# Optimization experiments

Measured on AMD Instinct MI355X. Metric: run time of the kernel, lower is better.

The kernel has to match this reference:

```python
import jax, jax.numpy as jnp
import numpy as np
from jax import lax

B, T, H = 32768, 64, 16
VOCAB_USER = 600001
VOCAB_LAUNCH = 3


def setup_inputs() -> dict:
    key = jax.random.key(0)
    ks = jax.random.split(key, 10)
    s = 1.0 / np.sqrt(H)
    return {
        "user_id": jax.random.randint(ks[0], (B,), 0, VOCAB_USER),
        "launch_seq": jax.random.randint(ks[1], (B, T), 0, VOCAB_LAUNCH),
        "user_emb": jax.random.normal(ks[2], (VOCAB_USER, H), dtype=jnp.float32),
        "launch_emb": jax.random.normal(ks[3], (VOCAB_LAUNCH, H), dtype=jnp.float32),
        "W_ih": jax.random.uniform(ks[4], (3 * H, H), jnp.float32, -s, s),
        "W_hh": jax.random.uniform(ks[5], (3 * H, H), jnp.float32, -s, s),
        "b_ih": jax.random.uniform(ks[6], (3 * H,), jnp.float32, -s, s),
        "b_hh": jax.random.uniform(ks[7], (3 * H,), jnp.float32, -s, s),
        "fc_W": jax.random.uniform(ks[8], (1, 2 * H), jnp.float32, -s, s),
        "fc_b": jax.random.uniform(ks[9], (1,), jnp.float32, -s, s),
    }


def reference(user_id, launch_seq, user_emb, launch_emb, W_ih, W_hh, b_ih, b_hh, fc_W, fc_b):
    u = user_emb[user_id]                      # (B, H)
    x = launch_emb[launch_seq]                 # (B, T, H)
    # precompute input contributions to the gates for all timesteps
    gx_all = jnp.einsum('bth,gh->btg', x, W_ih) + b_ih  # (B, T, 3H)

    def step(h, gx):
        gh = h @ W_hh.T + b_hh                 # (B, 3H)
        r = jax.nn.sigmoid(gx[:, :H] + gh[:, :H])
        z = jax.nn.sigmoid(gx[:, H:2 * H] + gh[:, H:2 * H])
        n = jnp.tanh(gx[:, 2 * H:] + r * gh[:, 2 * H:])
        h_new = (1.0 - z) * n + z * h
        return h_new, h_new

    h0 = jnp.zeros((x.shape[0], H), dtype=x.dtype)
    _, hs = lax.scan(step, h0, jnp.swapaxes(gx_all, 0, 1))  # hs: (T, B, H)
    pooled = jnp.mean(hs, axis=0)              # (B, H)
    fc_in = jnp.concatenate([u, pooled], axis=1)  # (B, 2H)
    return fc_in @ fc_W.T + fc_b               # (B, 1)
```

## Files before the change

kernel.cpp:

```cpp
#include <hip/hip_runtime.h>
#include <hip/hip_bf16.h>
#include <string.h>


#define NBLK 1024

typedef __attribute__((ext_vector_type(8)))  short    short8;
typedef __attribute__((ext_vector_type(16))) float    floatx16;
typedef __attribute__((ext_vector_type(4)))  unsigned uintx4;

static __device__ __forceinline__ float fexp2(float x) { return __builtin_amdgcn_exp2f(x); }
static __device__ __forceinline__ float frcp(float x)  { return __builtin_amdgcn_rcpf(x); }
static __device__ __forceinline__ unsigned short bfrne(float f) {
    union { __hip_bfloat16 b; unsigned short u; } cv; cv.b = __float2bfloat16(f); return cv.u;
}
static __device__ __forceinline__ float bf2f(unsigned short u) {
    unsigned v = ((unsigned)u) << 16; float f; memcpy(&f, &v, 4); return f;
}
static __device__ __forceinline__ unsigned pkbf(float a, float b) {
    return (unsigned)bfrne(a) | ((unsigned)bfrne(b) << 16);
}
static __device__ __forceinline__ float sel3(int c, float a0, float a1, float a2) {
    return c == 0 ? a0 : (c == 1 ? a1 : a2);
}

__global__ __launch_bounds__(64) void gru_mfma32(
    const int* __restrict__ user_id,
    const int* __restrict__ launch_seq,
    const float* __restrict__ user_emb,
    const float* __restrict__ launch_emb,
    const float* __restrict__ W_ih,
    const float* __restrict__ W_hh,
    const float* __restrict__ b_ih,
    const float* __restrict__ b_hh,
    const float* __restrict__ fc_W,
    const float* __restrict__ fc_b,
    float* __restrict__ out)
{
    constexpr float L  = 1.4426950408889634f;
    constexpr float L2 = 2.8853900817779268f;

    __shared__ float gxlut[144];

    const int tid  = threadIdx.x;
    const int n    = tid & 31;
    const int half = tid >> 5;
    const int d1o  = 4 * half;
    const long long sampBase = (long long)blockIdx.x * 32;

    unsigned pk[4];
    {
        const int* sp = launch_seq + (sampBase + n) * 64;
        #pragma unroll
        for (int w = 0; w < 4; ++w) {
            unsigned p = 0;
            #pragma unroll
            for (int j = 0; j < 4; ++j) {
                int4 v = ((const int4*)sp)[w * 4 + j];
                p |= ((unsigned)v.x & 3u) << (2 * (4 * j + 0));
                p |= ((unsigned)v.y & 3u) << (2 * (4 * j + 1));
                p |= ((unsigned)v.z & 3u) << (2 * (4 * j + 2));
                p |= ((unsigned)v.w & 3u) << (2 * (4 * j + 3));
            }
            pk[w] = p;
        }
    }

    for (int idx = tid; idx < 144; idx += 64) {
        int s = idx / 48, g = idx - s * 48;
        float dot = b_ih[g];
        #pragma unroll
        for (int k = 0; k < 16; ++k)
            dot = fmaf(W_ih[g * 16 + k], launch_emb[s * 16 + k], dot);
        int gate = g >> 4, dim = g & 15;
        gxlut[(gate * 3 + s) * 16 + dim] =
            (g < 32) ? (-L * (dot + b_hh[g])) : (L2 * dot);
    }

    short8 Arzh, Arzl, Anh, Anl;
    {
        auto split8 = [&](const float* w, short8& Hi, short8& Lo) {
            uintx4 hi, lo;
            #pragma unroll
            for (int p = 0; p < 4; ++p) {
                unsigned short h0 = bfrne(w[2 * p]), h1 = bfrne(w[2 * p + 1]);
                hi[p] = (unsigned)h0 | ((unsigned)h1 << 16);
                lo[p] = pkbf(w[2 * p] - bf2f(h0), w[2 * p + 1] - bf2f(h1));
            }
            Hi = __builtin_bit_cast(short8, hi);
            Lo = __builtin_bit_cast(short8, lo);
        };
        float w[8];
        const float* rowrz = W_hh + n * 16;
        float4 a = *(const float4*)(rowrz + d1o);
        float4 b = *(const float4*)(rowrz + d1o + 8);
        w[0] = -L * a.x; w[1] = -L * a.y; w[2] = -L * a.z; w[3] = -L * a.w;
        w[4] = -L * b.x; w[5] = -L * b.y; w[6] = -L * b.z; w[7] = -L * b.w;
        split8(w, Arzh, Arzl);
        if (n < 16) {
            const float* rown = W_hh + (32 + n) * 16;
            a = *(const float4*)(rown + d1o);
            b = *(const float4*)(rown + d1o + 8);
            w[0] = L2 * a.x; w[1] = L2 * a.y; w[2] = L2 * a.z; w[3] = L2 * a.w;
            w[4] = L2 * b.x; w[5] = L2 * b.y; w[6] = L2 * b.z; w[7] = L2 * b.w;
        } else {
            #pragma unroll
            for (int j = 0; j < 8; ++j) w[j] = 0.f;
        }
        split8(w, Anh, Anl);
    }

    float biasn[8];
    {
        float4 a = *(const float4*)&b_hh[32 + d1o];
        float4 b = *(const float4*)&b_hh[32 + d1o + 8];
        biasn[0] = L2 * a.x; biasn[1] = L2 * a.y; biasn[2] = L2 * a.z; biasn[3] = L2 * a.w;
        biasn[4] = L2 * b.x; biasn[5] = L2 * b.y; biasn[6] = L2 * b.z; biasn[7] = L2 * b.w;
    }

    __syncthreads();

    float gxr[3][8], gxz[3][8], gxn[3][8];
    #pragma unroll
    for (int c = 0; c < 3; ++c) {
        #pragma unroll
        for (int gbl = 0; gbl < 2; ++gbl) {
            int off = d1o + 8 * gbl;
            float4 r4 = *(const float4*)&gxlut[(0 * 3 + c) * 16 + off];
            float4 z4 = *(const float4*)&gxlut[(1 * 3 + c) * 16 + off];
            float4 n4 = *(const float4*)&gxlut[(2 * 3 + c) * 16 + off];
            gxr[c][4 * gbl + 0] = r4.x; gxr[c][4 * gbl + 1] = r4.y;
            gxr[c][4 * gbl + 2] = r4.z; gxr[c][4 * gbl + 3] = r4.w;
            gxz[c][4 * gbl + 0] = z4.x; gxz[c][4 * gbl + 1] = z4.y;
            gxz[c][4 * gbl + 2] = z4.z; gxz[c][4 * gbl + 3] = z4.w;
            gxn[c][4 * gbl + 0] = n4.x; gxn[c][4 * gbl + 1] = n4.y;
            gxn[c][4 * gbl + 2] = n4.z; gxn[c][4 * gbl + 3] = n4.w;
        }
    }

    floatx16 CZ;
    #pragma unroll
    for (int i = 0; i < 16; ++i) CZ[i] = 0.f;

    float h[8], pool[8];
    #pragma unroll
    for (int j = 0; j < 8; ++j) { h[j] = 0.f; pool[j] = 0.f; }
    short8 B = {0, 0, 0, 0, 0, 0, 0, 0};

    #pragma unroll
    for (int w = 0; w < 4; ++w) {
        unsigned cw = pk[w];
        #pragma unroll
        for (int tt = 0; tt < 16; ++tt) {
            int c = (int)(cw & 3u);
            cw >>= 2;

            floatx16 drz = __builtin_amdgcn_mfma_f32_32x32x16_bf16(Arzh, B, CZ, 0, 0, 0);
            floatx16 dn  = __builtin_amdgcn_mfma_f32_32x32x16_bf16(Anh,  B, CZ, 0, 0, 0);
            drz = __builtin_amdgcn_mfma_f32_32x32x16_bf16(Arzl, B, drz, 0, 0, 0);
            dn  = __builtin_amdgcn_mfma_f32_32x32x16_bf16(Anl,  B, dn,  0, 0, 0);

            #pragma unroll
            for (int j = 0; j < 8; ++j) {
                float gr = sel3(c, gxr[0][j], gxr[1][j], gxr[2][j]);
                float gz = sel3(c, gxz[0][j], gxz[1][j], gxz[2][j]);
                float gn = sel3(c, gxn[0][j], gxn[1][j], gxn[2][j]);
                float r  = frcp(1.0f + fexp2(drz[j] + gr));
                float z  = frcp(1.0f + fexp2(drz[8 + j] + gz));
                float y  = fmaf(r, dn[j] + biasn[j], gn);
                float nn = fmaf(-2.0f, frcp(1.0f + fexp2(y)), 1.0f);
                h[j] = fmaf(z, h[j] - nn, nn);
                pool[j] += h[j];
            }
            uintx4 b;
            b[0] = pkbf(h[0], h[1]);
            b[1] = pkbf(h[2], h[3]);
            b[2] = pkbf(h[4], h[5]);
            b[3] = pkbf(h[6], h[7]);
            B = __builtin_bit_cast(short8, b);
        }
    }

    float4 f1a = *(const float4*)&fc_W[d1o];
    float4 f1b = *(const float4*)&fc_W[d1o + 8];
    float4 f2a = *(const float4*)&fc_W[16 + d1o];
    float4 f2b = *(const float4*)&fc_W[16 + d1o + 8];
    int uid = user_id[sampBase + n];
    float4 ua = *(const float4*)&user_emb[(long long)uid * 16 + d1o];
    float4 ub = *(const float4*)&user_emb[(long long)uid * 16 + d1o + 8];
    const float inv64 = 1.0f / 64.0f;
    float val = f1a.x * ua.x + f1a.y * ua.y + f1a.z * ua.z + f1a.w * ua.w
              + f1b.x * ub.x + f1b.y * ub.y + f1b.z * ub.z + f1b.w * ub.w;
    val = fmaf(f2a.x * inv64, pool[0], val);
    val = fmaf(f2a.y * inv64, pool[1], val);
    val = fmaf(f2a.z * inv64, pool[2], val);
    val = fmaf(f2a.w * inv64, pool[3], val);
    val = fmaf(f2b.x * inv64, pool[4], val);
    val = fmaf(f2b.y * inv64, pool[5], val);
    val = fmaf(f2b.z * inv64, pool[6], val);
    val = fmaf(f2b.w * inv64, pool[7], val);
    val += __shfl_xor(val, 32);
    if (half == 0) out[sampBase + n] = val + fc_b[0];
}

extern "C" void kernel_launch(void* const* d_in, const int* in_sizes, int n_in,
                              void* d_out, int out_size, void* d_ws, size_t ws_size,
                              hipStream_t stream) {
    const int*   user_id    = (const int*)d_in[0];
    const int*   launch_seq = (const int*)d_in[1];
    const float* user_emb   = (const float*)d_in[2];
    const float* launch_emb = (const float*)d_in[3];
    const float* W_ih       = (const float*)d_in[4];
    const float* W_hh       = (const float*)d_in[5];
    const float* b_ih       = (const float*)d_in[6];
    const float* b_hh       = (const float*)d_in[7];
    const float* fc_W       = (const float*)d_in[8];
    const float* fc_b       = (const float*)d_in[9];
    float* out = (float*)d_out;

    gru_mfma32<<<dim3(NBLK), dim3(64), 0, stream>>>(
        user_id, launch_seq, user_emb, launch_emb,
        W_ih, W_hh, b_ih, b_hh, fc_W, fc_b, out);
}
```

Baseline: 134.2 us.

## Fold gate input terms into MFMA via one-hot B and drop bf16 lo-split

Removes the hi/lo bf16 split of W_hh, cutting the recurrent matrix work from four MFMAs to two per step. The per-step r/z input-gate contributions are produced by an extra MFMA that multiplies a small table (bf16 hi+lo) by a one-hot B operand selecting the launch token, and that result feeds as the accumulator of the Arz MFMA. The n-gate bias moves into the MFMA accumulator, and bf16 packing of h becomes cheaper round-half-up plus v_perm instead of RNE conversion. Dropping the lo correction lowers the precision of the recurrent matmul, and the one-hot MFMA adds a dependent MFMA to the chain before drz.

```diff
diff --git a/kernel.cpp b/kernel.cpp
--- a/kernel.cpp
+++ b/kernel.cpp
@@ -11,16 +11,22 @@
 
 static __device__ __forceinline__ float fexp2(float x) { return __builtin_amdgcn_exp2f(x); }
 static __device__ __forceinline__ float frcp(float x)  { return __builtin_amdgcn_rcpf(x); }
+static __device__ __forceinline__ unsigned f2u(float f) { unsigned u; memcpy(&u, &f, 4); return u; }
 static __device__ __forceinline__ unsigned short bfrne(float f) {
     union { __hip_bfloat16 b; unsigned short u; } cv; cv.b = __float2bfloat16(f); return cv.u;
 }
 static __device__ __forceinline__ float bf2f(unsigned short u) {
     unsigned v = ((unsigned)u) << 16; float f; memcpy(&f, &v, 4); return f;
 }
-static __device__ __forceinline__ unsigned pkbf(float a, float b) {
-    return (unsigned)bfrne(a) | ((unsigned)bfrne(b) << 16);
-}
-static __device__ __forceinline__ float sel3(int c, float a0, float a1, float a2) {
+static __device__ __forceinline__ unsigned pkrnd(float a, float b) {
+    unsigned ua = f2u(a) + 0x8000u;
+    unsigned ub = f2u(b) + 0x8000u;
+    return __builtin_amdgcn_perm(ub, ua, 0x07060302u);
+}
+static __device__ __forceinline__ float sel3f(int c, float a0, float a1, float a2) {
+    return c == 0 ? a0 : (c == 1 ? a1 : a2);
+}
+static __device__ __forceinline__ unsigned sel3u(int c, unsigned a0, unsigned a1, unsigned a2) {
     return c == 0 ? a0 : (c == 1 ? a1 : a2);
 }
 
@@ -77,18 +83,14 @@
             (g < 32) ? (-L * (dot + b_hh[g])) : (L2 * dot);
     }
 
-    short8 Arzh, Arzl, Anh, Anl;
-    {
-        auto split8 = [&](const float* w, short8& Hi, short8& Lo) {
-            uintx4 hi, lo;
-            #pragma unroll
-            for (int p = 0; p < 4; ++p) {
-                unsigned short h0 = bfrne(w[2 * p]), h1 = bfrne(w[2 * p + 1]);
-                hi[p] = (unsigned)h0 | ((unsigned)h1 << 16);
-                lo[p] = pkbf(w[2 * p] - bf2f(h0), w[2 * p + 1] - bf2f(h1));
-            }
-            Hi = __builtin_bit_cast(short8, hi);
-            Lo = __builtin_bit_cast(short8, lo);
+    short8 Arz, An;
+    {
+        auto pack8 = [&](const float* w) {
+            uintx4 hi;
+            #pragma unroll
+            for (int p = 0; p < 4; ++p)
+                hi[p] = (unsigned)bfrne(w[2 * p]) | ((unsigned)bfrne(w[2 * p + 1]) << 16);
+            return __builtin_bit_cast(short8, hi);
         };
         float w[8];
         const float* rowrz = W_hh + n * 16;
@@ -96,7 +98,7 @@
         float4 b = *(const float4*)(rowrz + d1o + 8);
         w[0] = -L * a.x; w[1] = -L * a.y; w[2] = -L * a.z; w[3] = -L * a.w;
         w[4] = -L * b.x; w[5] = -L * b.y; w[6] = -L * b.z; w[7] = -L * b.w;
-        split8(w, Arzh, Arzl);
+        Arz = pack8(w);
         if (n < 16) {
             const float* rown = W_hh + (32 + n) * 16;
             a = *(const float4*)(rown + d1o);
@@ -107,35 +109,48 @@
             #pragma unroll
             for (int j = 0; j < 8; ++j) w[j] = 0.f;
         }
-        split8(w, Anh, Anl);
-    }
-
-    float biasn[8];
+        An = pack8(w);
+    }
+
+    __syncthreads();
+
+    short8 Agx;
+    {
+        uintx4 d = {0u, 0u, 0u, 0u};
+        if (half == 0) {
+            const float* base = (n < 16) ? &gxlut[0] : &gxlut[48];
+            int dim = n & 15;
+            float g0 = base[0 * 16 + dim];
+            float g1 = base[1 * 16 + dim];
+            float g2 = base[2 * 16 + dim];
+            unsigned short h0 = bfrne(g0), h1 = bfrne(g1), h2 = bfrne(g2);
+            d[0] = (unsigned)h0 | ((unsigned)h1 << 16);
+            d[1] = (unsigned)h2 | ((unsigned)bfrne(g0 - bf2f(h0)) << 16);
+            d[2] = (unsigned)bfrne(g1 - bf2f(h1)) | ((unsigned)bfrne(g2 - bf2f(h2)) << 16);
+        }
+        Agx = __builtin_bit_cast(short8, d);
+    }
+
+    const unsigned khA = half ? 0u : 0x3F80u;
+    const unsigned khB = half ? 0u : 0x3F800000u;
+
+    floatx16 Cn;
+    #pragma unroll
+    for (int i = 0; i < 16; ++i) Cn[i] = 0.f;
     {
         float4 a = *(const float4*)&b_hh[32 + d1o];
         float4 b = *(const float4*)&b_hh[32 + d1o + 8];
-        biasn[0] = L2 * a.x; biasn[1] = L2 * a.y; biasn[2] = L2 * a.z; biasn[3] = L2 * a.w;
-        biasn[4] = L2 * b.x; biasn[5] = L2 * b.y; biasn[6] = L2 * b.z; biasn[7] = L2 * b.w;
-    }
-
-    __syncthreads();
-
-    float gxr[3][8], gxz[3][8], gxn[3][8];
+        Cn[0] = L2 * a.x; Cn[1] = L2 * a.y; Cn[2] = L2 * a.z; Cn[3] = L2 * a.w;
+        Cn[4] = L2 * b.x; Cn[5] = L2 * b.y; Cn[6] = L2 * b.z; Cn[7] = L2 * b.w;
+    }
+
+    float gxn[3][8];
     #pragma unroll
     for (int c = 0; c < 3; ++c) {
-        #pragma unroll
-        for (int gbl = 0; gbl < 2; ++gbl) {
-            int off = d1o + 8 * gbl;
-            float4 r4 = *(const float4*)&gxlut[(0 * 3 + c) * 16 + off];
-            float4 z4 = *(const float4*)&gxlut[(1 * 3 + c) * 16 + off];
-            float4 n4 = *(const float4*)&gxlut[(2 * 3 + c) * 16 + off];
-            gxr[c][4 * gbl + 0] = r4.x; gxr[c][4 * gbl + 1] = r4.y;
-            gxr[c][4 * gbl + 2] = r4.z; gxr[c][4 * gbl + 3] = r4.w;
-            gxz[c][4 * gbl + 0] = z4.x; gxz[c][4 * gbl + 1] = z4.y;
-            gxz[c][4 * gbl + 2] = z4.z; gxz[c][4 * gbl + 3] = z4.w;
-            gxn[c][4 * gbl + 0] = n4.x; gxn[c][4 * gbl + 1] = n4.y;
-            gxn[c][4 * gbl + 2] = n4.z; gxn[c][4 * gbl + 3] = n4.w;
-        }
+        float4 a = *(const float4*)&gxlut[(6 + c) * 16 + d1o];
+        float4 b = *(const float4*)&gxlut[(6 + c) * 16 + d1o + 8];
+        gxn[c][0] = a.x; gxn[c][1] = a.y; gxn[c][2] = a.z; gxn[c][3] = a.w;
+        gxn[c][4] = b.x; gxn[c][5] = b.y; gxn[c][6] = b.z; gxn[c][7] = b.w;
     }
 
     floatx16 CZ;
@@ -147,37 +162,51 @@
     for (int j = 0; j < 8; ++j) { h[j] = 0.f; pool[j] = 0.f; }
     short8 B = {0, 0, 0, 0, 0, 0, 0, 0};
 
+    short8 Bp;
+    {
+        int c0 = (int)(pk[0] & 3u);
+        uintx4 bp = { sel3u(c0, khA, khB, 0u),
+                      sel3u(c0, khB, 0u, khA),
+                      sel3u(c0, 0u, khA, khB), 0u };
+        Bp = __builtin_bit_cast(short8, bp);
+    }
+
     #pragma unroll
     for (int w = 0; w < 4; ++w) {
-        unsigned cw = pk[w];
+        unsigned cw  = pk[w];
+        unsigned ncw = (pk[w] >> 2) | (w < 3 ? (pk[w + 1] << 30) : 0u);
         #pragma unroll
         for (int tt = 0; tt < 16; ++tt) {
             int c = (int)(cw & 3u);
-            cw >>= 2;
-
-            floatx16 drz = __builtin_amdgcn_mfma_f32_32x32x16_bf16(Arzh, B, CZ, 0, 0, 0);
-            floatx16 dn  = __builtin_amdgcn_mfma_f32_32x32x16_bf16(Anh,  B, CZ, 0, 0, 0);
-            drz = __builtin_amdgcn_mfma_f32_32x32x16_bf16(Arzl, B, drz, 0, 0, 0);
-            dn  = __builtin_amdgcn_mfma_f32_32x32x16_bf16(Anl,  B, dn,  0, 0, 0);
+
+            floatx16 t1  = __builtin_amdgcn_mfma_f32_32x32x16_bf16(Agx, Bp, CZ, 0, 0, 0);
+            floatx16 dn  = __builtin_amdgcn_mfma_f32_32x32x16_bf16(An,  B, Cn, 0, 0, 0);
+            floatx16 drz = __builtin_amdgcn_mfma_f32_32x32x16_bf16(Arz, B, t1, 0, 0, 0);
 
             #pragma unroll
             for (int j = 0; j < 8; ++j) {
-                float gr = sel3(c, gxr[0][j], gxr[1][j], gxr[2][j]);
-                float gz = sel3(c, gxz[0][j], gxz[1][j], gxz[2][j]);
-                float gn = sel3(c, gxn[0][j], gxn[1][j], gxn[2][j]);
-                float r  = frcp(1.0f + fexp2(drz[j] + gr));
-                float z  = frcp(1.0f + fexp2(drz[8 + j] + gz));
-                float y  = fmaf(r, dn[j] + biasn[j], gn);
+                float gn = sel3f(c, gxn[0][j], gxn[1][j], gxn[2][j]);
+                float r  = frcp(1.0f + fexp2(drz[j]));
+                float z  = frcp(1.0f + fexp2(drz[8 + j]));
+                float y  = fmaf(r, dn[j], gn);
                 float nn = fmaf(-2.0f, frcp(1.0f + fexp2(y)), 1.0f);
                 h[j] = fmaf(z, h[j] - nn, nn);
                 pool[j] += h[j];
             }
+
+            int cn = (int)(ncw & 3u);
+            uintx4 bp = { sel3u(cn, khA, khB, 0u),
+                          sel3u(cn, khB, 0u, khA),
+                          sel3u(cn, 0u, khA, khB), 0u };
+            Bp = __builtin_bit_cast(short8, bp);
             uintx4 b;
-            b[0] = pkbf(h[0], h[1]);
-            b[1] = pkbf(h[2], h[3]);
-            b[2] = pkbf(h[4], h[5]);
-            b[3] = pkbf(h[6], h[7]);
+            b[0] = pkrnd(h[0], h[1]);
+            b[1] = pkrnd(h[2], h[3]);
+            b[2] = pkrnd(h[4], h[5]);
+            b[3] = pkrnd(h[6], h[7]);
             B = __builtin_bit_cast(short8, b);
+            cw >>= 2;
+            ncw >>= 2;
         }
     }
 
```

Result: faster. 126.6 us (-5.7%).
